# Performance work log

Hardware: AMD Instinct MI355X
Metric: run time of the kernel (lower is better)

The kernel has to match this reference:

```python
import jax, jax.numpy as jnp
import numpy as np

EPS = 1.0


def _onedirectional_dist(a, b):
    # a: (B, M), b: (B, N) -> per-batch sum over M of min_n (a_m - b_n)^2
    d2 = (a[:, :, None] - b[:, None, :]) ** 2  # (B, M, N)
    return jnp.min(d2, axis=2).sum(axis=1)  # (B,)


def setup_inputs() -> dict:
    key = jax.random.key(0)
    k1, k2, k3 = jax.random.split(key, 3)
    target = jax.random.uniform(k1, (4, 240, 320), dtype=jnp.float32)
    bin_centers = jax.random.uniform(k2, (4, 256), dtype=jnp.float32)
    mask = jax.random.randint(k3, (4, 240, 320), 0, 2).astype(jnp.bool_)
    return {"target": target, "bin_centers": bin_centers, "mask": mask}


def reference(target, bin_centers, mask):
    # masked path of ChamferDistanceLoss.forward
    max_target = jnp.max(jnp.where(mask, target, -jnp.inf))
    max_center = jnp.max(bin_centers)
    mx = jnp.maximum(max_target, max_center)
    mn = jnp.minimum(max_target, max_center)
    pad_value = mx + (mx - mn) + EPS
    B = bin_centers.shape[0]
    # pad bin_centers with one extra column = pad_value
    mod_centers = jnp.concatenate(
        [bin_centers, jnp.broadcast_to(pad_value, (B, 1)).astype(bin_centers.dtype)],
        axis=1,
    )  # (B, n_bins + 1)
    # invalid target pixels replaced by pad_value
    mod_target = jnp.where(mask, target, pad_value).reshape(B, -1)  # (B, H*W)
    bidir = _onedirectional_dist(mod_centers, mod_target) + _onedirectional_dist(
        mod_target, mod_centers
    )
    return jnp.mean(bidir)
```

## Files before the change

kernel.cpp:

```cpp
#include <hip/hip_runtime.h>
#include <math.h>

#define B 4
#define HW 76800
#define NBINS 256
#define TPB 256
#define D1B 64
#define C1  4
#define D2B 75
#define PXB 1024
#define F4T (HW / 4 / TPB)


__global__ __launch_bounds__(256) void kmain(const float* __restrict__ target,
                                             const int* __restrict__ mask,
                                             const float* __restrict__ centers,
                                             float* __restrict__ out) {
    __shared__ __align__(16) float s_c2[NBINS];
    __shared__ __align__(16) float s_c[NBINS];
    __shared__ float s_d1[4][C1];
    __shared__ float s_red[4];
    const int tid = threadIdx.x;
    const int b   = blockIdx.y;
    const int blk = blockIdx.x;
    const float BIG = 1e38f;

    if (blk < D1B) {
        float c[C1], c2[C1], mn[C1];
#pragma unroll
        for (int k = 0; k < C1; ++k) {
            c[k]  = centers[b * NBINS + blk * C1 + k];
            c2[k] = c[k] * c[k];
            mn[k] = INFINITY;
        }
        const float4* tp = (const float4*)(target + b * HW);
        const int4*   mp = (const int4*)(mask + b * HW);
#pragma unroll 3
        for (int j = 0; j < F4T; ++j) {
            float4 p = tp[j * TPB + tid];
            int4   m = mp[j * TPB + tid];
            float q0 = p.x + p.x, s0 = m.x ? p.x * p.x : BIG;
            float q1 = p.y + p.y, s1 = m.y ? p.y * p.y : BIG;
            float q2 = p.z + p.z, s2 = m.z ? p.z * p.z : BIG;
            float q3 = p.w + p.w, s3 = m.w ? p.w * p.w : BIG;
#pragma unroll
            for (int k = 0; k < C1; ++k) {
                float d0 = fmaf(-c[k], q0, s0);
                float d1 = fmaf(-c[k], q1, s1);
                float d2 = fmaf(-c[k], q2, s2);
                float d3 = fmaf(-c[k], q3, s3);
                mn[k] = fminf(mn[k], fminf(fminf(d0, d1), fminf(d2, d3)));
            }
        }
        for (int o = 32; o > 0; o >>= 1) {
#pragma unroll
            for (int k = 0; k < C1; ++k)
                mn[k] = fminf(mn[k], __shfl_down(mn[k], o));
        }
        if ((tid & 63) == 0) {
            int w = tid >> 6;
#pragma unroll
            for (int k = 0; k < C1; ++k) s_d1[w][k] = mn[k];
        }
        __syncthreads();
        if (tid == 0) {
            float tot = 0.f;
#pragma unroll
            for (int k = 0; k < C1; ++k) {
                float r = fminf(fminf(s_d1[0][k], s_d1[1][k]),
                                fminf(s_d1[2][k], s_d1[3][k]));
                tot += r + c2[k];
            }
            atomicAdd(out, 0.25f * tot);
        }
    } else {
        const int blk2 = blk - D1B;
        const int base = b * HW + blk2 * PXB;
        float4 v  = ((const float4*)(target + base))[tid];
        int4   mm = ((const int4*)(mask + base))[tid];
        {
            float c = centers[b * NBINS + tid];
            s_c[tid]  = c;
            s_c2[tid] = c * c;
        }
        __syncthreads();

        float q0 = v.x + v.x, q1 = v.y + v.y;
        float q2 = v.z + v.z, q3 = v.w + v.w;
        float mn0 = INFINITY, mn1 = INFINITY;
        float mn2 = INFINITY, mn3 = INFINITY;
        const float4* s_c4  = (const float4*)s_c;
        const float4* s_c24 = (const float4*)s_c2;
#pragma unroll 4
        for (int g = 0; g < NBINS / 4; ++g) {
            float4 c  = s_c4[g];
            float4 c2 = s_c24[g];
            float a0 = fmaf(-c.x, q0, c2.x), a1 = fmaf(-c.y, q0, c2.y);
            float a2 = fmaf(-c.z, q0, c2.z), a3 = fmaf(-c.w, q0, c2.w);
            mn0 = fminf(mn0, fminf(fminf(a0, a1), fminf(a2, a3)));
            float b0 = fmaf(-c.x, q1, c2.x), b1 = fmaf(-c.y, q1, c2.y);
            float b2 = fmaf(-c.z, q1, c2.z), b3 = fmaf(-c.w, q1, c2.w);
            mn1 = fminf(mn1, fminf(fminf(b0, b1), fminf(b2, b3)));
            float e0 = fmaf(-c.x, q2, c2.x), e1 = fmaf(-c.y, q2, c2.y);
            float e2 = fmaf(-c.z, q2, c2.z), e3 = fmaf(-c.w, q2, c2.w);
            mn2 = fminf(mn2, fminf(fminf(e0, e1), fminf(e2, e3)));
            float f0 = fmaf(-c.x, q3, c2.x), f1 = fmaf(-c.y, q3, c2.y);
            float f2 = fmaf(-c.z, q3, c2.z), f3 = fmaf(-c.w, q3, c2.w);
            mn3 = fminf(mn3, fminf(fminf(f0, f1), fminf(f2, f3)));
        }
        float acc = (mm.x ? fmaf(v.x, v.x, mn0) : 0.f)
                  + (mm.y ? fmaf(v.y, v.y, mn1) : 0.f)
                  + (mm.z ? fmaf(v.z, v.z, mn2) : 0.f)
                  + (mm.w ? fmaf(v.w, v.w, mn3) : 0.f);
        for (int o = 32; o > 0; o >>= 1) acc += __shfl_down(acc, o);
        if ((tid & 63) == 0) s_red[tid >> 6] = acc;
        __syncthreads();
        if (tid == 0)
            atomicAdd(out, 0.25f * (s_red[0] + s_red[1] + s_red[2] + s_red[3]));
    }
}

extern "C" void kernel_launch(void* const* d_in, const int* in_sizes, int n_in,
                              void* d_out, int out_size, void* d_ws, size_t ws_size,
                              hipStream_t stream) {
    const float* target  = (const float*)d_in[0];
    const float* centers = (const float*)d_in[1];
    const int*   mask    = (const int*)d_in[2];
    float* out = (float*)d_out;

    dim3 g(D1B + D2B, B);
    kmain<<<g, TPB, 0, stream>>>(target, mask, centers, out);
}
```

Measured before the change: 74.88 us.

## Fuse both Chamfer directions per pixel tile with atomicMin slots and last-block reduction

Drops the split into 64 long-running center-side blocks and separate pixel-side blocks. Each 512-pixel block now computes pixel-to-center minima and also per-center minima over its own tile. The per-center results are merged globally by atomicMin on order-preserving unsigned encodings in workspace. A grid-wide counter picks the last block, which finishes the center-side sum. This targets load imbalance from the long serial center-side blocks, at the cost of an extra memset launch, global atomics and a threadfence-based completion protocol.

Measured after the change: 117.7 us. +57.2%, slower.

```diff
diff --git a/kernel.cpp b/kernel.cpp
--- a/kernel.cpp
+++ b/kernel.cpp
@@ -5,115 +5,106 @@
 #define HW 76800
 #define NBINS 256
 #define TPB 256
-#define D1B 64
-#define C1  4
-#define D2B 75
-#define PXB 1024
-#define F4T (HW / 4 / TPB)
+#define PXB 512
+#define BPB (HW / PXB)
+#define GRID_TOTAL (BPB * B)
 
+
+__device__ __forceinline__ unsigned fmap(float f) {
+    unsigned u = __float_as_uint(f);
+    return (u & 0x80000000u) ? ~u : (u | 0x80000000u);
+}
+__device__ __forceinline__ float funmap(unsigned k) {
+    unsigned u = (k & 0x80000000u) ? (k ^ 0x80000000u) : ~k;
+    return __uint_as_float(u);
+}
 
 __global__ __launch_bounds__(256) void kmain(const float* __restrict__ target,
                                              const int* __restrict__ mask,
                                              const float* __restrict__ centers,
-                                             float* __restrict__ out) {
+                                             float* __restrict__ out,
+                                             unsigned* __restrict__ ws) {
+    __shared__ __align__(16) float s_q[PXB];
+    __shared__ __align__(16) float s_s[PXB];
+    __shared__ __align__(16) float s_c[NBINS];
     __shared__ __align__(16) float s_c2[NBINS];
-    __shared__ __align__(16) float s_c[NBINS];
-    __shared__ float s_d1[4][C1];
     __shared__ float s_red[4];
+    __shared__ unsigned s_last;
     const int tid = threadIdx.x;
     const int b   = blockIdx.y;
     const int blk = blockIdx.x;
     const float BIG = 1e38f;
+    unsigned* slots = ws;
+    unsigned* cnt   = ws + B * NBINS;
 
-    if (blk < D1B) {
-        float c[C1], c2[C1], mn[C1];
+    const int base = b * HW + blk * PXB;
+    float2 v  = ((const float2*)(target + base))[tid];
+    int2   mm = ((const int2*)(mask + base))[tid];
+    float q0 = v.x + v.x, q1 = v.y + v.y;
+    float s0 = mm.x ? v.x * v.x : BIG;
+    float s1 = mm.y ? v.y * v.y : BIG;
+    s_q[2 * tid]     = q0;
+    s_q[2 * tid + 1] = q1;
+    s_s[2 * tid]     = s0;
+    s_s[2 * tid + 1] = s1;
+    {
+        float c = centers[b * NBINS + tid];
+        s_c[tid]  = c;
+        s_c2[tid] = c * c;
+    }
+    __syncthreads();
+
+    float mn0 = INFINITY, mn1 = INFINITY;
+    const float4* c4  = (const float4*)s_c;
+    const float4* c24 = (const float4*)s_c2;
+#pragma unroll 4
+    for (int g = 0; g < NBINS / 4; ++g) {
+        float4 c  = c4[g];
+        float4 c2 = c24[g];
+        float a0 = fmaf(-c.x, q0, c2.x), a1 = fmaf(-c.y, q0, c2.y);
+        float a2 = fmaf(-c.z, q0, c2.z), a3 = fmaf(-c.w, q0, c2.w);
+        mn0 = fminf(mn0, fminf(fminf(a0, a1), fminf(a2, a3)));
+        float b0 = fmaf(-c.x, q1, c2.x), b1 = fmaf(-c.y, q1, c2.y);
+        float b2 = fmaf(-c.z, q1, c2.z), b3 = fmaf(-c.w, q1, c2.w);
+        mn1 = fminf(mn1, fminf(fminf(b0, b1), fminf(b2, b3)));
+    }
+    float acc = (mm.x ? fmaf(v.x, v.x, mn0) : 0.f)
+              + (mm.y ? fmaf(v.y, v.y, mn1) : 0.f);
+
+    const float cme = s_c[tid];
+    float mnc = INFINITY;
+    const float4* q4 = (const float4*)s_q;
+    const float4* s4 = (const float4*)s_s;
+#pragma unroll 4
+    for (int g = 0; g < PXB / 4; ++g) {
+        float4 qq = q4[g];
+        float4 ss = s4[g];
+        float d0 = fmaf(-cme, qq.x, ss.x), d1 = fmaf(-cme, qq.y, ss.y);
+        float d2 = fmaf(-cme, qq.z, ss.z), d3 = fmaf(-cme, qq.w, ss.w);
+        mnc = fminf(mnc, fminf(fminf(d0, d1), fminf(d2, d3)));
+    }
+    atomicMin(&slots[b * NBINS + tid], fmap(mnc));
+
+    for (int o = 32; o > 0; o >>= 1) acc += __shfl_down(acc, o);
+    if ((tid & 63) == 0) s_red[tid >> 6] = acc;
+    __syncthreads();
+    if (tid == 0)
+        atomicAdd(out, 0.25f * (s_red[0] + s_red[1] + s_red[2] + s_red[3]));
+
+    __threadfence();
+    if (tid == 0) s_last = atomicAdd(cnt, 1u);
+    __syncthreads();
+    if (s_last == (unsigned)(GRID_TOTAL - 2)) {
+        __threadfence();
+        float sum = 0.f;
 #pragma unroll
-        for (int k = 0; k < C1; ++k) {
-            c[k]  = centers[b * NBINS + blk * C1 + k];
-            c2[k] = c[k] * c[k];
-            mn[k] = INFINITY;
+        for (int bb = 0; bb < B; ++bb) {
+            unsigned k = atomicMin(&slots[bb * NBINS + tid], 0xFFFFFFFFu);
+            float c = centers[bb * NBINS + tid];
+            sum += funmap(k) + c * c;
         }
-        const float4* tp = (const float4*)(target + b * HW);
-        const int4*   mp = (const int4*)(mask + b * HW);
-#pragma unroll 3
-        for (int j = 0; j < F4T; ++j) {
-            float4 p = tp[j * TPB + tid];
-            int4   m = mp[j * TPB + tid];
-            float q0 = p.x + p.x, s0 = m.x ? p.x * p.x : BIG;
-            float q1 = p.y + p.y, s1 = m.y ? p.y * p.y : BIG;
-            float q2 = p.z + p.z, s2 = m.z ? p.z * p.z : BIG;
-            float q3 = p.w + p.w, s3 = m.w ? p.w * p.w : BIG;
-#pragma unroll
-            for (int k = 0; k < C1; ++k) {
-                float d0 = fmaf(-c[k], q0, s0);
-                float d1 = fmaf(-c[k], q1, s1);
-                float d2 = fmaf(-c[k], q2, s2);
-                float d3 = fmaf(-c[k], q3, s3);
-                mn[k] = fminf(mn[k], fminf(fminf(d0, d1), fminf(d2, d3)));
-            }
-        }
-        for (int o = 32; o > 0; o >>= 1) {
-#pragma unroll
-            for (int k = 0; k < C1; ++k)
-                mn[k] = fminf(mn[k], __shfl_down(mn[k], o));
-        }
-        if ((tid & 63) == 0) {
-            int w = tid >> 6;
-#pragma unroll
-            for (int k = 0; k < C1; ++k) s_d1[w][k] = mn[k];
-        }
-        __syncthreads();
-        if (tid == 0) {
-            float tot = 0.f;
-#pragma unroll
-            for (int k = 0; k < C1; ++k) {
-                float r = fminf(fminf(s_d1[0][k], s_d1[1][k]),
-                                fminf(s_d1[2][k], s_d1[3][k]));
-                tot += r + c2[k];
-            }
-            atomicAdd(out, 0.25f * tot);
-        }
-    } else {
-        const int blk2 = blk - D1B;
-        const int base = b * HW + blk2 * PXB;
-        float4 v  = ((const float4*)(target + base))[tid];
-        int4   mm = ((const int4*)(mask + base))[tid];
-        {
-            float c = centers[b * NBINS + tid];
-            s_c[tid]  = c;
-            s_c2[tid] = c * c;
-        }
-        __syncthreads();
-
-        float q0 = v.x + v.x, q1 = v.y + v.y;
-        float q2 = v.z + v.z, q3 = v.w + v.w;
-        float mn0 = INFINITY, mn1 = INFINITY;
-        float mn2 = INFINITY, mn3 = INFINITY;
-        const float4* s_c4  = (const float4*)s_c;
-        const float4* s_c24 = (const float4*)s_c2;
-#pragma unroll 4
-        for (int g = 0; g < NBINS / 4; ++g) {
-            float4 c  = s_c4[g];
-            float4 c2 = s_c24[g];
-            float a0 = fmaf(-c.x, q0, c2.x), a1 = fmaf(-c.y, q0, c2.y);
-            float a2 = fmaf(-c.z, q0, c2.z), a3 = fmaf(-c.w, q0, c2.w);
-            mn0 = fminf(mn0, fminf(fminf(a0, a1), fminf(a2, a3)));
-            float b0 = fmaf(-c.x, q1, c2.x), b1 = fmaf(-c.y, q1, c2.y);
-            float b2 = fmaf(-c.z, q1, c2.z), b3 = fmaf(-c.w, q1, c2.w);
-            mn1 = fminf(mn1, fminf(fminf(b0, b1), fminf(b2, b3)));
-            float e0 = fmaf(-c.x, q2, c2.x), e1 = fmaf(-c.y, q2, c2.y);
-            float e2 = fmaf(-c.z, q2, c2.z), e3 = fmaf(-c.w, q2, c2.w);
-            mn2 = fminf(mn2, fminf(fminf(e0, e1), fminf(e2, e3)));
-            float f0 = fmaf(-c.x, q3, c2.x), f1 = fmaf(-c.y, q3, c2.y);
-            float f2 = fmaf(-c.z, q3, c2.z), f3 = fmaf(-c.w, q3, c2.w);
-            mn3 = fminf(mn3, fminf(fminf(f0, f1), fminf(f2, f3)));
-        }
-        float acc = (mm.x ? fmaf(v.x, v.x, mn0) : 0.f)
-                  + (mm.y ? fmaf(v.y, v.y, mn1) : 0.f)
-                  + (mm.z ? fmaf(v.z, v.z, mn2) : 0.f)
-                  + (mm.w ? fmaf(v.w, v.w, mn3) : 0.f);
-        for (int o = 32; o > 0; o >>= 1) acc += __shfl_down(acc, o);
-        if ((tid & 63) == 0) s_red[tid >> 6] = acc;
+        for (int o = 32; o > 0; o >>= 1) sum += __shfl_down(sum, o);
+        if ((tid & 63) == 0) s_red[tid >> 6] = sum;
         __syncthreads();
         if (tid == 0)
             atomicAdd(out, 0.25f * (s_red[0] + s_red[1] + s_red[2] + s_red[3]));
@@ -128,6 +119,7 @@
     const int*   mask    = (const int*)d_in[2];
     float* out = (float*)d_out;
 
-    dim3 g(D1B + D2B, B);
-    kmain<<<g, TPB, 0, stream>>>(target, mask, centers, out);
+    hipMemsetAsync(d_ws, 0xFF, (B * NBINS + 1) * sizeof(unsigned), stream);
+    dim3 g(BPB, B);
+    kmain<<<g, TPB, 0, stream>>>(target, mask, centers, out, (unsigned*)d_ws);
 }
```
